# Optimization experiments

Hardware: AMD Instinct MI355X
Metric: run time of the kernel (lower is better)

The kernel has to match this reference:

```python
import jax, jax.numpy as jnp
import numpy as np


def _conv1x1(W, x):
    # W: [out, in], x: [B, in, D, H, W] -> [B, out, D, H, W]
    return jnp.einsum('oc,bcdhw->bodhw', W, x)


def _maxpool2(x):
    # 2x2x2 max pool, stride 2, over the last three (spatial) dims
    return jax.lax.reduce_window(x, -jnp.inf, jax.lax.max,
                                 (1, 1, 2, 2, 2), (1, 1, 2, 2, 2), 'VALID')


def setup_inputs() -> dict:
    key = jax.random.key(0)
    ks = jax.random.split(key, 5)
    B, C, D, H, W = 4, 256, 24, 24, 24
    Cq = C // 8
    x = jax.random.normal(ks[0], (B, C, D, H, W), dtype=jnp.float32)
    Wf = jax.random.normal(ks[1], (Cq, C), dtype=jnp.float32) * (C ** -0.5)
    Wg = jax.random.normal(ks[2], (Cq, C), dtype=jnp.float32) * (C ** -0.5)
    Wh = jax.random.normal(ks[3], (Cq, C), dtype=jnp.float32) * (C ** -0.5)
    Wv = jax.random.normal(ks[4], (C, Cq), dtype=jnp.float32) * (Cq ** -0.5)
    gamma = jnp.ones((), dtype=jnp.float32)
    return {"x": x, "Wf": Wf, "Wg": Wg, "Wh": Wh, "Wv": Wv, "gamma": gamma}


def reference(x, Wf, Wg, Wh, Wv, gamma):
    B, C, D, H, W = x.shape
    Cq = Wf.shape[0]
    N = D * H * W          # query length
    M = N // 8

    f = _conv1x1(Wf, x).reshape(B, Cq, N)                 # [B, Cq, N]
    g = _maxpool2(_conv1x1(Wg, x)).reshape(B, Cq, M)      # [B, Cq, M]
    h = _maxpool2(_conv1x1(Wh, x)).reshape(B, Cq, M)      # [B, Cq, M]

    scores = jnp.einsum('bcn,bcm->bnm', f, g)             # [B, N, M]
    beta = jax.nn.softmax(scores, axis=-1)
    o = jnp.einsum('bcm,bnm->bcn', h, beta)               # [B, Cq, N]
    o = _conv1x1(Wv, o.reshape(B, Cq, D, H, W))           # [B, C, D, H, W]
    return gamma * o + x
```

## Files before the change

### kernel.cpp

```cpp
#include <hip/hip_runtime.h>

#define B 4
#define C 256
#define CQ 32
#define NN 13824
#define MM 1728
#define MS 12

typedef __attribute__((ext_vector_type(8))) short short8;
typedef __attribute__((ext_vector_type(4))) float float4_;
typedef __attribute__((ext_vector_type(16))) float floatx16;

static __device__ inline unsigned rne_bf16(float x) {
  unsigned u = __float_as_uint(x);
  u += 0x7FFFu + ((u >> 16) & 1u);
  return u >> 16;
}

__global__ __launch_bounds__(256) void wcvt_kernel(
    const float* __restrict__ Wf, const float* __restrict__ Wg,
    const float* __restrict__ Wh, unsigned short* __restrict__ W16c) {
  const int i = blockIdx.x * 256 + threadIdx.x;
  const int kk = i & 7;
  const int rest = i >> 3;
  const int m = rest % 96;
  const int r = rest / 96;
  const int kq = r & 3;
  const int ch = r >> 2;
  const int k = ch * 32 + kq * 8 + kk;
  const float* Wr = (m < 32) ? (Wf + m * C) : (m < 64) ? (Wg + (m - 32) * C)
                                                       : (Wh + (m - 64) * C);
  W16c[i] = (unsigned short)rne_bf16(Wr[k]);
}

__global__ __launch_bounds__(256) void proj_mfma(
    const float* __restrict__ x, const unsigned short* __restrict__ W16c,
    unsigned short* __restrict__ f16, unsigned short* __restrict__ g16,
    unsigned short* __restrict__ h16) {
  __shared__ __align__(16) unsigned short xls[2][4][128][8];
  __shared__ __align__(16) unsigned short wls[2][4][96][8];
  const int blk = blockIdx.x;
  const int b = blk / 108;
  const int n0 = (blk - b * 108) * 128;
  const int t = threadIdx.x;
  const int w = t >> 6, lane = t & 63;
  const int col = lane & 31, hi = lane >> 5;
  const int sn = t & 127, sh = t >> 7;

  floatx16 accf = {0}, accg = {0}, acch = {0};

  {
    const float* xp = x + ((size_t)b * C) * NN + n0 + sn;
#pragma unroll
    for (int it = 0; it < 2; ++it) {
      const int kq = sh * 2 + it;
      float v[8];
#pragma unroll
      for (int kk = 0; kk < 8; ++kk) v[kk] = xp[(size_t)(kq * 8 + kk) * NN];
      *reinterpret_cast<uint4*>(&xls[0][kq][sn][0]) =
          make_uint4(rne_bf16(v[0]) | (rne_bf16(v[1]) << 16),
                     rne_bf16(v[2]) | (rne_bf16(v[3]) << 16),
                     rne_bf16(v[4]) | (rne_bf16(v[5]) << 16),
                     rne_bf16(v[6]) | (rne_bf16(v[7]) << 16));
    }
    const uint4* src = reinterpret_cast<const uint4*>(W16c);
    uint4* dst = reinterpret_cast<uint4*>(&wls[0][0][0][0]);
    dst[t] = src[t];
    if (t < 128) dst[256 + t] = src[256 + t];
  }
  __syncthreads();

  for (int ch = 0; ch < 8; ++ch) {
    const int buf = ch & 1;
    if (ch < 7) {
      const float* xp = x + ((size_t)b * C + (ch + 1) * 32) * NN + n0 + sn;
#pragma unroll
      for (int it = 0; it < 2; ++it) {
        const int kq = sh * 2 + it;
        float v[8];
#pragma unroll
        for (int kk = 0; kk < 8; ++kk) v[kk] = xp[(size_t)(kq * 8 + kk) * NN];
        *reinterpret_cast<uint4*>(&xls[buf ^ 1][kq][sn][0]) =
            make_uint4(rne_bf16(v[0]) | (rne_bf16(v[1]) << 16),
                       rne_bf16(v[2]) | (rne_bf16(v[3]) << 16),
                       rne_bf16(v[4]) | (rne_bf16(v[5]) << 16),
                       rne_bf16(v[6]) | (rne_bf16(v[7]) << 16));
      }
      const uint4* src =
          reinterpret_cast<const uint4*>(W16c + (size_t)(ch + 1) * 3072);
      uint4* dst = reinterpret_cast<uint4*>(&wls[buf ^ 1][0][0][0]);
      dst[t] = src[t];
      if (t < 128) dst[256 + t] = src[256 + t];
    }
#pragma unroll
    for (int ks = 0; ks < 2; ++ks) {
      const int kq = ks * 2 + hi;
      const short8 bfr = *reinterpret_cast<const short8*>(&xls[buf][kq][w * 32 + col][0]);
      const short8 a0 = *reinterpret_cast<const short8*>(&wls[buf][kq][col][0]);
      const short8 a1 = *reinterpret_cast<const short8*>(&wls[buf][kq][32 + col][0]);
      const short8 a2 = *reinterpret_cast<const short8*>(&wls[buf][kq][64 + col][0]);
      accf = __builtin_amdgcn_mfma_f32_32x32x16_bf16(a0, bfr, accf, 0, 0, 0);
      accg = __builtin_amdgcn_mfma_f32_32x32x16_bf16(a1, bfr, accg, 0, 0, 0);
      acch = __builtin_amdgcn_mfma_f32_32x32x16_bf16(a2, bfr, acch, 0, 0, 0);
    }
    __syncthreads();
  }

  const int n = n0 + w * 32 + col;
  {
    unsigned short* fp = f16 + ((size_t)b * NN + n) * 32 + hi * 4;
#pragma unroll
    for (int rp = 0; rp < 8; ++rp) {
      const int m = (rp & 1) * 2 + 8 * (rp >> 1);
      *reinterpret_cast<unsigned*>(fp + m) =
          rne_bf16(accf[rp * 2]) | (rne_bf16(accf[rp * 2 + 1]) << 16);
    }
  }
  unsigned short* gp = g16 + (size_t)b * CQ * NN + n;
  unsigned short* hp = h16 + (size_t)b * CQ * NN + n;
#pragma unroll
  for (int r = 0; r < 16; ++r) {
    const int c = (r & 3) + 8 * (r >> 2) + 4 * hi;
    gp[(size_t)c * NN] = (unsigned short)rne_bf16(accg[r]);
    hp[(size_t)c * NN] = (unsigned short)rne_bf16(acch[r]);
  }
}

__global__ __launch_bounds__(256) void pool_kernel(
    const unsigned short* __restrict__ g16, const unsigned short* __restrict__ h16,
    unsigned short* __restrict__ gt16, unsigned short* __restrict__ ht16) {
  int i = blockIdx.x * 256 + threadIdx.x;
  const int c = i & 31;
  const int rest = i >> 5;
  const int m = rest % MM;
  const int b = rest / MM;
  const int wq = m % MS;
  const int hq = (m / MS) % MS;
  const int dq = m / (MS * MS);
  const size_t base = ((size_t)b * CQ + c) * NN +
                      (2 * dq) * 576 + (2 * hq) * 24 + (2 * wq);
  auto mx2 = [](unsigned u) {
    return fmaxf(__uint_as_float(u << 16), __uint_as_float(u & 0xFFFF0000u));
  };
  const unsigned short* pg = g16 + base;
  const unsigned short* ph = h16 + base;
  float vg = fmaxf(fmaxf(mx2(*(const unsigned*)(pg)),
                         mx2(*(const unsigned*)(pg + 24))),
                   fmaxf(mx2(*(const unsigned*)(pg + 576)),
                         mx2(*(const unsigned*)(pg + 600))));
  float vh = fmaxf(fmaxf(mx2(*(const unsigned*)(ph)),
                         mx2(*(const unsigned*)(ph + 24))),
                   fmaxf(mx2(*(const unsigned*)(ph + 576)),
                         mx2(*(const unsigned*)(ph + 600))));
  gt16[((size_t)b * MM + m) * 32 + c] = (unsigned short)(__float_as_uint(vg) >> 16);
  ht16[((size_t)b * 32 + c) * MM + m] = (unsigned short)(__float_as_uint(vh) >> 16);
}

__global__ __launch_bounds__(256, 4) void attn_kernel(
    const unsigned short* __restrict__ f16, const unsigned short* __restrict__ gt,
    const unsigned short* __restrict__ ht, const float* __restrict__ x,
    const float* __restrict__ Wv, const float* __restrict__ gamma,
    float* __restrict__ out) {
  __shared__ __align__(16) unsigned short sm[16896];
  const int blk = blockIdx.x;
  const int b = blk / 216;
  const int n0 = (blk - b * 216) * 64;
  const int t = threadIdx.x;
  const int w = t >> 6, L = t & 63, Q = L >> 4, col = L & 15;

  unsigned short* fls = sm;
  unsigned short* g0 = sm + 2560;
  unsigned short* g1 = sm + 5120;
  unsigned short* h0 = sm + 7680;
  unsigned short* h1 = sm + 9984;
  unsigned short* Pls = sm + 12288 + w * 1152;

  {
    const unsigned short* fsrc = f16 + ((size_t)(b * NN + n0)) * 32;
    *reinterpret_cast<uint4*>(fls + (t >> 2) * 40 + (t & 3) * 8) =
        *reinterpret_cast<const uint4*>(fsrc + t * 8);
  }
  const unsigned short* gsrc = gt + (size_t)b * MM * 32;
  const unsigned short* hsrc = ht + (size_t)b * 32 * MM;
  const int gk = t >> 2, gseg = t & 3;
  const int hc = t >> 3, hseg = t & 7;
  *reinterpret_cast<uint4*>(g0 + gk * 40 + gseg * 8) =
      *reinterpret_cast<const uint4*>(gsrc + gk * 32 + gseg * 8);
  *reinterpret_cast<uint4*>(h0 + hc * 72 + hseg * 8) =
      *reinterpret_cast<const uint4*>(hsrc + (size_t)hc * MM + hseg * 8);
  __syncthreads();

  const short8 fB = *reinterpret_cast<const short8*>(fls + (w * 16 + col) * 40 + Q * 8);

  float4_ acc0 = {0.f, 0.f, 0.f, 0.f}, acc1 = {0.f, 0.f, 0.f, 0.f};
  float l = 0.f;

  for (int ch = 0; ch < 27; ++ch) {
    unsigned short* gcur = (ch & 1) ? g1 : g0;
    unsigned short* hcur = (ch & 1) ? h1 : h0;
    uint4 gnx, hnx;
    if (ch < 26) {
      const int k0 = (ch + 1) * 64;
      gnx = *reinterpret_cast<const uint4*>(gsrc + (size_t)(k0 + gk) * 32 + gseg * 8);
      hnx = *reinterpret_cast<const uint4*>(hsrc + (size_t)hc * MM + k0 + hseg * 8);
    }
    float4_ sc[4];
#pragma unroll
    for (int T = 0; T < 4; ++T) {
      const short8 gA =
          *reinterpret_cast<const short8*>(gcur + (T * 16 + col) * 40 + Q * 8);
      float4_ z = {0.f, 0.f, 0.f, 0.f};
      sc[T] = __builtin_amdgcn_mfma_f32_16x16x32_bf16(gA, fB, z, 0, 0, 0);
    }
#pragma unroll
    for (int T = 0; T < 4; ++T) {
      const float p0 = __expf(sc[T][0] - 30.f);
      const float p1 = __expf(sc[T][1] - 30.f);
      const float p2 = __expf(sc[T][2] - 30.f);
      const float p3 = __expf(sc[T][3] - 30.f);
      l += (p0 + p1) + (p2 + p3);
      unsigned short* pw = Pls + col * 72 + T * 16 + Q * 4;
      *reinterpret_cast<uint2*>(pw) =
          make_uint2(rne_bf16(p0) | (rne_bf16(p1) << 16),
                     rne_bf16(p2) | (rne_bf16(p3) << 16));
    }
#pragma unroll
    for (int ks = 0; ks < 2; ++ks) {
      const short8 pA =
          *reinterpret_cast<const short8*>(Pls + col * 72 + ks * 32 + Q * 8);
      const short8 hB0 =
          *reinterpret_cast<const short8*>(hcur + col * 72 + ks * 32 + Q * 8);
      const short8 hB1 =
          *reinterpret_cast<const short8*>(hcur + (16 + col) * 72 + ks * 32 + Q * 8);
      acc0 = __builtin_amdgcn_mfma_f32_16x16x32_bf16(pA, hB0, acc0, 0, 0, 0);
      acc1 = __builtin_amdgcn_mfma_f32_16x16x32_bf16(pA, hB1, acc1, 0, 0, 0);
    }
    if (ch < 26) {
      unsigned short* gnb = (ch & 1) ? g0 : g1;
      unsigned short* hnb = (ch & 1) ? h0 : h1;
      *reinterpret_cast<uint4*>(gnb + gk * 40 + gseg * 8) = gnx;
      *reinterpret_cast<uint4*>(hnb + hc * 72 + hseg * 8) = hnx;
    }
    __syncthreads();
  }

  l += __shfl_xor(l, 16);
  l += __shfl_xor(l, 32);
  float* ols = reinterpret_cast<float*>(sm);
#pragma unroll
  for (int r = 0; r < 4; ++r) {
    const float linv = 1.f / __shfl(l, Q * 4 + r);
    const int nl = w * 16 + Q * 4 + r;
    ols[nl * 33 + col] = acc0[r] * linv;
    ols[nl * 33 + 16 + col] = acc1[r] * linv;
  }
  __syncthreads();

  const int nl = t & 63;
  const int cg = __builtin_amdgcn_readfirstlane(t >> 6);
  float ov[CQ];
#pragma unroll
  for (int q = 0; q < CQ; ++q) ov[q] = ols[nl * 33 + q];
  const float gm = gamma[0];
  const float* xb = x + ((size_t)b * C + cg * 64) * NN + n0 + nl;
  float* ob = out + ((size_t)b * C + cg * 64) * NN + n0 + nl;
  float xv[8];
#pragma unroll
  for (int j = 0; j < 8; ++j) xv[j] = xb[(size_t)j * NN];
#pragma unroll
  for (int cc = 0; cc < 64; cc += 8) {
    float xn[8];
    if (cc < 56) {
#pragma unroll
      for (int j = 0; j < 8; ++j) xn[j] = xb[(size_t)(cc + 8 + j) * NN];
    }
#pragma unroll
    for (int j = 0; j < 8; ++j) {
      const float* wr = Wv + (cg * 64 + cc + j) * CQ;
      float s = 0.f;
#pragma unroll
      for (int q = 0; q < CQ; ++q) s = fmaf(wr[q], ov[q], s);
      ob[(size_t)(cc + j) * NN] = gm * s + xv[j];
    }
    if (cc < 56) {
#pragma unroll
      for (int j = 0; j < 8; ++j) xv[j] = xn[j];
    }
  }
}

extern "C" void kernel_launch(void* const* d_in, const int* in_sizes, int n_in,
                              void* d_out, int out_size, void* d_ws, size_t ws_size,
                              hipStream_t stream) {
  const float* x     = (const float*)d_in[0];
  const float* Wf    = (const float*)d_in[1];
  const float* Wg    = (const float*)d_in[2];
  const float* Wh    = (const float*)d_in[3];
  const float* Wv    = (const float*)d_in[4];
  const float* gamma = (const float*)d_in[5];
  float* out = (float*)d_out;
  float* ws = (float*)d_ws;

  unsigned short* f16  = (unsigned short*)ws;
  unsigned short* g16  = (unsigned short*)(ws + 884736);
  unsigned short* h16  = (unsigned short*)(ws + 1769472);
  unsigned short* gt16 = (unsigned short*)(ws + 4423680);
  unsigned short* ht16 = (unsigned short*)(ws + 4534272);
  unsigned short* W16c = (unsigned short*)(ws + 4644864);

  wcvt_kernel<<<96, 256, 0, stream>>>(Wf, Wg, Wh, W16c);
  proj_mfma<<<B * 108, 256, 0, stream>>>(x, W16c, f16, g16, h16);
  pool_kernel<<<(B * CQ * MM) / 256, 256, 0, stream>>>(g16, h16, gt16, ht16);
  attn_kernel<<<B * (NN / 64), 256, 0, stream>>>(f16, gt16, ht16, x, Wv, gamma, out);
}
```

Baseline: 187.1 us.

## Use MFMA with split-bf16 Wv for output projection and deepen proj prefetch

The attention epilogue's scalar 32-wide FMA output projection is replaced by bf16 MFMA. Wv is pre-split into high and low bf16 parts by the weight-conversion kernel to keep some precision, while the attention output itself is rounded to bf16. The projection kernel is restructured to prefetch x two chunks ahead into registers and W one chunk ahead, separating global loads from LDS stores so load latency overlaps with compute. This costs more registers and adds bf16 rounding error to the attention output.

Result: faster. 167.8 us (-10.3%).

```diff
diff --git a/kernel.cpp b/kernel.cpp
--- a/kernel.cpp
+++ b/kernel.cpp
@@ -19,19 +19,79 @@
 
 __global__ __launch_bounds__(256) void wcvt_kernel(
     const float* __restrict__ Wf, const float* __restrict__ Wg,
-    const float* __restrict__ Wh, unsigned short* __restrict__ W16c) {
+    const float* __restrict__ Wh, const float* __restrict__ Wv,
+    unsigned short* __restrict__ W16c, unsigned short* __restrict__ Whv,
+    unsigned short* __restrict__ Wlv) {
   const int i = blockIdx.x * 256 + threadIdx.x;
-  const int kk = i & 7;
-  const int rest = i >> 3;
-  const int m = rest % 96;
-  const int r = rest / 96;
-  const int kq = r & 3;
-  const int ch = r >> 2;
-  const int k = ch * 32 + kq * 8 + kk;
-  const float* Wr = (m < 32) ? (Wf + m * C) : (m < 64) ? (Wg + (m - 32) * C)
-                                                       : (Wh + (m - 64) * C);
-  W16c[i] = (unsigned short)rne_bf16(Wr[k]);
-}
+  if (i < 24576) {
+    const int kk = i & 7;
+    const int rest = i >> 3;
+    const int m = rest % 96;
+    const int r = rest / 96;
+    const int kq = r & 3;
+    const int ch = r >> 2;
+    const int k = ch * 32 + kq * 8 + kk;
+    const float* Wr = (m < 32) ? (Wf + m * C) : (m < 64) ? (Wg + (m - 32) * C)
+                                                         : (Wh + (m - 64) * C);
+    W16c[i] = (unsigned short)rne_bf16(Wr[k]);
+  } else {
+    const int j = i - 24576;
+    const float v = Wv[j];
+    const unsigned h = rne_bf16(v);
+    Whv[j] = (unsigned short)h;
+    Wlv[j] = (unsigned short)rne_bf16(v - __uint_as_float(h << 16));
+  }
+}
+
+#define LOADX(SET, CH)                                                        \
+  do {                                                                        \
+    const float* xp = xbase + (size_t)((CH)*32) * NN;                         \
+    _Pragma("unroll") for (int it = 0; it < 2; ++it) {                        \
+      _Pragma("unroll") for (int kk = 0; kk < 8; ++kk)                        \
+          vx[SET][it][kk] = xp[(size_t)((sh * 2 + it) * 8 + kk) * NN];        \
+    }                                                                         \
+  } while (0)
+
+#define PACKX(SET, BUF)                                                       \
+  do {                                                                        \
+    _Pragma("unroll") for (int it = 0; it < 2; ++it) {                        \
+      const int kq = sh * 2 + it;                                             \
+      *reinterpret_cast<uint4*>(&xls[BUF][kq][sn][0]) = make_uint4(           \
+          rne_bf16(vx[SET][it][0]) | (rne_bf16(vx[SET][it][1]) << 16),        \
+          rne_bf16(vx[SET][it][2]) | (rne_bf16(vx[SET][it][3]) << 16),        \
+          rne_bf16(vx[SET][it][4]) | (rne_bf16(vx[SET][it][5]) << 16),        \
+          rne_bf16(vx[SET][it][6]) | (rne_bf16(vx[SET][it][7]) << 16));       \
+    }                                                                         \
+  } while (0)
+
+#define LOADW(CH)                                                             \
+  do {                                                                        \
+    const uint4* src = reinterpret_cast<const uint4*>(W16c + (size_t)(CH)*3072); \
+    wr0 = src[t];                                                             \
+    if (t < 128) wr1 = src[256 + t];                                          \
+  } while (0)
+
+#define STOREW(BUF)                                                           \
+  do {                                                                        \
+    uint4* dst = reinterpret_cast<uint4*>(&wls[BUF][0][0][0]);                \
+    dst[t] = wr0;                                                             \
+    if (t < 128) dst[256 + t] = wr1;                                          \
+  } while (0)
+
+#define COMPUTE(BUF)                                                          \
+  do {                                                                        \
+    _Pragma("unroll") for (int ks = 0; ks < 2; ++ks) {                        \
+      const int kq = ks * 2 + hi;                                             \
+      const short8 bfr =                                                      \
+          *reinterpret_cast<const short8*>(&xls[BUF][kq][w * 32 + col][0]);   \
+      const short8 a0 = *reinterpret_cast<const short8*>(&wls[BUF][kq][col][0]);      \
+      const short8 a1 = *reinterpret_cast<const short8*>(&wls[BUF][kq][32 + col][0]); \
+      const short8 a2 = *reinterpret_cast<const short8*>(&wls[BUF][kq][64 + col][0]); \
+      accf = __builtin_amdgcn_mfma_f32_32x32x16_bf16(a0, bfr, accf, 0, 0, 0); \
+      accg = __builtin_amdgcn_mfma_f32_32x32x16_bf16(a1, bfr, accg, 0, 0, 0); \
+      acch = __builtin_amdgcn_mfma_f32_32x32x16_bf16(a2, bfr, acch, 0, 0, 0); \
+    }                                                                         \
+  } while (0)
 
 __global__ __launch_bounds__(256) void proj_mfma(
     const float* __restrict__ x, const unsigned short* __restrict__ W16c,
@@ -48,62 +108,30 @@
   const int sn = t & 127, sh = t >> 7;
 
   floatx16 accf = {0}, accg = {0}, acch = {0};
-
-  {
-    const float* xp = x + ((size_t)b * C) * NN + n0 + sn;
-#pragma unroll
-    for (int it = 0; it < 2; ++it) {
-      const int kq = sh * 2 + it;
-      float v[8];
-#pragma unroll
-      for (int kk = 0; kk < 8; ++kk) v[kk] = xp[(size_t)(kq * 8 + kk) * NN];
-      *reinterpret_cast<uint4*>(&xls[0][kq][sn][0]) =
-          make_uint4(rne_bf16(v[0]) | (rne_bf16(v[1]) << 16),
-                     rne_bf16(v[2]) | (rne_bf16(v[3]) << 16),
-                     rne_bf16(v[4]) | (rne_bf16(v[5]) << 16),
-                     rne_bf16(v[6]) | (rne_bf16(v[7]) << 16));
-    }
-    const uint4* src = reinterpret_cast<const uint4*>(W16c);
-    uint4* dst = reinterpret_cast<uint4*>(&wls[0][0][0][0]);
-    dst[t] = src[t];
-    if (t < 128) dst[256 + t] = src[256 + t];
-  }
+  const float* xbase = x + ((size_t)b * C) * NN + n0 + sn;
+  float vx[2][2][8];
+  uint4 wr0, wr1;
+
+  LOADX(0, 0);
+  PACKX(0, 0);
+  LOADW(0);
+  STOREW(0);
+  LOADX(1, 1);
   __syncthreads();
 
+#pragma unroll
   for (int ch = 0; ch < 8; ++ch) {
     const int buf = ch & 1;
-    if (ch < 7) {
-      const float* xp = x + ((size_t)b * C + (ch + 1) * 32) * NN + n0 + sn;
-#pragma unroll
-      for (int it = 0; it < 2; ++it) {
-        const int kq = sh * 2 + it;
-        float v[8];
-#pragma unroll
-        for (int kk = 0; kk < 8; ++kk) v[kk] = xp[(size_t)(kq * 8 + kk) * NN];
-        *reinterpret_cast<uint4*>(&xls[buf ^ 1][kq][sn][0]) =
-            make_uint4(rne_bf16(v[0]) | (rne_bf16(v[1]) << 16),
-                       rne_bf16(v[2]) | (rne_bf16(v[3]) << 16),
-                       rne_bf16(v[4]) | (rne_bf16(v[5]) << 16),
-                       rne_bf16(v[6]) | (rne_bf16(v[7]) << 16));
-      }
-      const uint4* src =
-          reinterpret_cast<const uint4*>(W16c + (size_t)(ch + 1) * 3072);
-      uint4* dst = reinterpret_cast<uint4*>(&wls[buf ^ 1][0][0][0]);
-      dst[t] = src[t];
-      if (t < 128) dst[256 + t] = src[256 + t];
-    }
-#pragma unroll
-    for (int ks = 0; ks < 2; ++ks) {
-      const int kq = ks * 2 + hi;
-      const short8 bfr = *reinterpret_cast<const short8*>(&xls[buf][kq][w * 32 + col][0]);
-      const short8 a0 = *reinterpret_cast<const short8*>(&wls[buf][kq][col][0]);
-      const short8 a1 = *reinterpret_cast<const short8*>(&wls[buf][kq][32 + col][0]);
-      const short8 a2 = *reinterpret_cast<const short8*>(&wls[buf][kq][64 + col][0]);
-      accf = __builtin_amdgcn_mfma_f32_32x32x16_bf16(a0, bfr, accf, 0, 0, 0);
-      accg = __builtin_amdgcn_mfma_f32_32x32x16_bf16(a1, bfr, accg, 0, 0, 0);
-      acch = __builtin_amdgcn_mfma_f32_32x32x16_bf16(a2, bfr, acch, 0, 0, 0);
-    }
-    __syncthreads();
+    if (ch + 1 < 8) LOADW(ch + 1);
+    if (ch + 2 < 8) {
+      if (buf == 0) LOADX(0, ch + 2); else LOADX(1, ch + 2);
+    }
+    COMPUTE(buf);
+    if (ch + 1 < 8) {
+      if (buf == 0) PACKX(1, 1); else PACKX(0, 0);
+      STOREW(buf ^ 1);
+      __syncthreads();
+    }
   }
 
   const int n = n0 + w * 32 + col;
@@ -159,8 +187,8 @@
 __global__ __launch_bounds__(256, 4) void attn_kernel(
     const unsigned short* __restrict__ f16, const unsigned short* __restrict__ gt,
     const unsigned short* __restrict__ ht, const float* __restrict__ x,
-    const float* __restrict__ Wv, const float* __restrict__ gamma,
-    float* __restrict__ out) {
+    const unsigned short* __restrict__ Whv, const unsigned short* __restrict__ Wlv,
+    const float* __restrict__ gamma, float* __restrict__ out) {
   __shared__ __align__(16) unsigned short sm[16896];
   const int blk = blockIdx.x;
   const int b = blk / 216;
@@ -256,35 +284,52 @@
   }
   __syncthreads();
 
-  const int nl = t & 63;
-  const int cg = __builtin_amdgcn_readfirstlane(t >> 6);
-  float ov[CQ];
-#pragma unroll
-  for (int q = 0; q < CQ; ++q) ov[q] = ols[nl * 33 + q];
+  const int colA = L & 31, hiA = L >> 5;
   const float gm = gamma[0];
-  const float* xb = x + ((size_t)b * C + cg * 64) * NN + n0 + nl;
-  float* ob = out + ((size_t)b * C + cg * 64) * NN + n0 + nl;
-  float xv[8];
-#pragma unroll
-  for (int j = 0; j < 8; ++j) xv[j] = xb[(size_t)j * NN];
-#pragma unroll
-  for (int cc = 0; cc < 64; cc += 8) {
-    float xn[8];
-    if (cc < 56) {
-#pragma unroll
-      for (int j = 0; j < 8; ++j) xn[j] = xb[(size_t)(cc + 8 + j) * NN];
-    }
-#pragma unroll
-    for (int j = 0; j < 8; ++j) {
-      const float* wr = Wv + (cg * 64 + cc + j) * CQ;
-      float s = 0.f;
-#pragma unroll
-      for (int q = 0; q < CQ; ++q) s = fmaf(wr[q], ov[q], s);
-      ob[(size_t)(cc + j) * NN] = gm * s + xv[j];
-    }
-    if (cc < 56) {
-#pragma unroll
-      for (int j = 0; j < 8; ++j) xv[j] = xn[j];
+  short8 Bf[2][2];
+#pragma unroll
+  for (int nt = 0; nt < 2; ++nt) {
+#pragma unroll
+    for (int ks = 0; ks < 2; ++ks) {
+      const float* p = &ols[(nt * 32 + colA) * 33 + ks * 16 + hiA * 8];
+      uint4 uu;
+      uu.x = rne_bf16(p[0]) | (rne_bf16(p[1]) << 16);
+      uu.y = rne_bf16(p[2]) | (rne_bf16(p[3]) << 16);
+      uu.z = rne_bf16(p[4]) | (rne_bf16(p[5]) << 16);
+      uu.w = rne_bf16(p[6]) | (rne_bf16(p[7]) << 16);
+      Bf[nt][ks] = *reinterpret_cast<short8*>(&uu);
+    }
+  }
+#pragma unroll
+  for (int tt = 0; tt < 2; ++tt) {
+    const int ct = w + tt * 4;
+    const int ca = ct * 32 + colA;
+    const short8 Ah0 = *reinterpret_cast<const short8*>(Whv + ca * 32 + hiA * 8);
+    const short8 Ah1 = *reinterpret_cast<const short8*>(Whv + ca * 32 + 16 + hiA * 8);
+    const short8 Al0 = *reinterpret_cast<const short8*>(Wlv + ca * 32 + hiA * 8);
+    const short8 Al1 = *reinterpret_cast<const short8*>(Wlv + ca * 32 + 16 + hiA * 8);
+    floatx16 ac0 = {0}, ac1 = {0};
+    ac0 = __builtin_amdgcn_mfma_f32_32x32x16_bf16(Ah0, Bf[0][0], ac0, 0, 0, 0);
+    ac0 = __builtin_amdgcn_mfma_f32_32x32x16_bf16(Ah1, Bf[0][1], ac0, 0, 0, 0);
+    ac0 = __builtin_amdgcn_mfma_f32_32x32x16_bf16(Al0, Bf[0][0], ac0, 0, 0, 0);
+    ac0 = __builtin_amdgcn_mfma_f32_32x32x16_bf16(Al1, Bf[0][1], ac0, 0, 0, 0);
+    ac1 = __builtin_amdgcn_mfma_f32_32x32x16_bf16(Ah0, Bf[1][0], ac1, 0, 0, 0);
+    ac1 = __builtin_amdgcn_mfma_f32_32x32x16_bf16(Ah1, Bf[1][1], ac1, 0, 0, 0);
+    ac1 = __builtin_amdgcn_mfma_f32_32x32x16_bf16(Al0, Bf[1][0], ac1, 0, 0, 0);
+    ac1 = __builtin_amdgcn_mfma_f32_32x32x16_bf16(Al1, Bf[1][1], ac1, 0, 0, 0);
+#pragma unroll
+    for (int nt = 0; nt < 2; ++nt) {
+      const floatx16 av = nt ? ac1 : ac0;
+      const int n = n0 + nt * 32 + colA;
+      const float* xp = x + ((size_t)b * C + ct * 32 + 4 * hiA) * NN + n;
+      float* op = out + ((size_t)b * C + ct * 32 + 4 * hiA) * NN + n;
+      float xv[16];
+#pragma unroll
+      for (int r = 0; r < 16; ++r)
+        xv[r] = xp[(size_t)((r & 3) + 8 * (r >> 2)) * NN];
+#pragma unroll
+      for (int r = 0; r < 16; ++r)
+        op[(size_t)((r & 3) + 8 * (r >> 2)) * NN] = gm * av[r] + xv[r];
     }
   }
 }
@@ -304,12 +349,15 @@
   unsigned short* f16  = (unsigned short*)ws;
   unsigned short* g16  = (unsigned short*)(ws + 884736);
   unsigned short* h16  = (unsigned short*)(ws + 1769472);
+  unsigned short* Whv  = (unsigned short*)(ws + 2654208);
+  unsigned short* Wlv  = (unsigned short*)(ws + 2658304);
   unsigned short* gt16 = (unsigned short*)(ws + 4423680);
   unsigned short* ht16 = (unsigned short*)(ws + 4534272);
   unsigned short* W16c = (unsigned short*)(ws + 4644864);
 
-  wcvt_kernel<<<96, 256, 0, stream>>>(Wf, Wg, Wh, W16c);
+  wcvt_kernel<<<128, 256, 0, stream>>>(Wf, Wg, Wh, Wv, W16c, Whv, Wlv);
   proj_mfma<<<B * 108, 256, 0, stream>>>(x, W16c, f16, g16, h16);
   pool_kernel<<<(B * CQ * MM) / 256, 256, 0, stream>>>(g16, h16, gt16, ht16);
-  attn_kernel<<<B * (NN / 64), 256, 0, stream>>>(f16, gt16, ht16, x, Wv, gamma, out);
-}
+  attn_kernel<<<B * (NN / 64), 256, 0, stream>>>(f16, gt16, ht16, x, Whv, Wlv,
+                                                 gamma, out);
+}
```
